# Optimization experiments

Hardware: AMD Instinct MI355X
Metric: run time of the kernel (lower is better)

The kernel has to match this reference:

```python
import jax, jax.numpy as jnp
import numpy as np

WINDOW = 4  # window_size
H = 8       # n_heads


def setup_inputs() -> dict:
    key = jax.random.key(0)
    ks = jax.random.split(key, 12)
    B, C, T = 4, 512, 1024
    d = C // H
    x = jax.random.normal(ks[0], (B, C, T), dtype=jnp.float32)
    mask = jnp.ones((B, 1, 1, T), dtype=jnp.int32)
    s = 0.02
    Wq = jax.random.normal(ks[1], (C, C), dtype=jnp.float32) * s
    Wk = jax.random.normal(ks[2], (C, C), dtype=jnp.float32) * s
    Wv = jax.random.normal(ks[3], (C, C), dtype=jnp.float32) * s
    Wo = jax.random.normal(ks[4], (C, C), dtype=jnp.float32) * s
    bq = jnp.zeros((C,), jnp.float32)
    bk = jnp.zeros((C,), jnp.float32)
    bv = jnp.zeros((C,), jnp.float32)
    bo = jnp.zeros((C,), jnp.float32)
    rel_std = d ** (-0.5)
    emb_rel_k = jax.random.normal(ks[5], (1, 2 * WINDOW + 1, d), dtype=jnp.float32) * rel_std
    emb_rel_v = jax.random.normal(ks[6], (1, 2 * WINDOW + 1, d), dtype=jnp.float32) * rel_std
    return {"x": x, "mask": mask, "Wq": Wq, "bq": bq, "Wk": Wk, "bk": bk,
            "Wv": Wv, "bv": bv, "Wo": Wo, "bo": bo,
            "emb_rel_k": emb_rel_k, "emb_rel_v": emb_rel_v}


def _slice_rel_emb(emb, T, pad_len, start, end):
    # F.pad(emb, [0,0,pad,pad,0,0]) then [:, start:end] -> [1, 2T-1, d]
    p = jnp.pad(emb, ((0, 0), (pad_len, pad_len), (0, 0)))
    return p[:, start:end]


def reference(x, mask, Wq, bq, Wk, bk, Wv, bv, Wo, bo, emb_rel_k, emb_rel_v):
    B, C, T = x.shape
    d = C // H
    scale = jnp.asarray(np.sqrt(d), x.dtype)

    def proj(Wm, bm):
        return jnp.einsum('oc,bct->bot', Wm, x) + bm[None, :, None]

    def to_heads(t):  # [B,C,T] -> [B,H,T,d]
        return t.reshape(B, H, d, T).transpose(0, 1, 3, 2)

    query = to_heads(proj(Wq, bq))
    key_ = to_heads(proj(Wk, bk))
    value = to_heads(proj(Wv, bv))

    score = jnp.einsum('bhtd,bhsd->bhts', query, key_) / scale

    pad_len = max(0, T - (WINDOW + 1))
    start = max(0, WINDOW + 1 - T)
    end = start + 2 * T - 1

    k_emb = _slice_rel_emb(emb_rel_k, T, pad_len, start, end)  # [1, 2T-1, d]
    rel = jnp.einsum('bhtd,rd->bhtr', query, k_emb[0])          # [B,H,T,2T-1]
    # skew trick: relative -> absolute
    rel = jnp.pad(rel, ((0, 0), (0, 0), (0, 0), (0, 1))).reshape(B, H, 2 * T * T)
    rel = jnp.pad(rel, ((0, 0), (0, 0), (0, T - 1))).reshape(B, H, T + 1, 2 * T - 1)
    score_loc = rel[:, :, :T, T - 1:] / scale
    score = score + score_loc

    score = jnp.where(mask == 0, jnp.asarray(-10000.0, score.dtype), score)
    p_attn = jax.nn.softmax(score, axis=-1)  # dropout=0 (eval)

    output = jnp.einsum('bhts,bhsd->bhtd', p_attn, value)

    # inverse skew: absolute -> relative weights [B,H,T,2T-1]
    pw = jnp.pad(p_attn, ((0, 0), (0, 0), (0, 0), (0, T - 1))).reshape(B, H, T * (2 * T - 1))
    pw = jnp.pad(pw, ((0, 0), (0, 0), (T, 0))).reshape(B, H, T, 2 * T)[:, :, :, 1:]
    v_emb = _slice_rel_emb(emb_rel_v, T, pad_len, start, end)  # [1, 2T-1, d]
    output = output + jnp.einsum('bhtr,rd->bhtd', pw, v_emb[0])

    out = output.transpose(0, 1, 3, 2).reshape(B, C, T)
    return jnp.einsum('oc,bct->bot', Wo, out) + bo[None, :, None]
```

## Files before the change

### kernel.cpp

```cpp
#include <hip/hip_runtime.h>

typedef unsigned short u16;
typedef unsigned int u32;
using f32x4 = __attribute__((ext_vector_type(4))) float;
using s16x8 = __attribute__((ext_vector_type(8))) short;
using u16x4 = __attribute__((ext_vector_type(4))) unsigned short;
using u16x8 = __attribute__((ext_vector_type(8))) unsigned short;

#define GLOAD_LDS16(g, s)                                     \
  __builtin_amdgcn_global_load_lds(                           \
      (const __attribute__((address_space(1))) void*)(g),     \
      (__attribute__((address_space(3))) void*)(s), 16, 0, 0)

namespace {

constexpr int T = 1024;
constexpr int C = 512;
constexpr float QSCALE = 0.125f * 1.4426950408889634f;
constexpr float MASKED = -14427.0f;
constexpr float DEFER_THR = 11.0f;

__device__ inline u16 f2bf(float f) {
  u32 u = __builtin_bit_cast(u32, f);
  u32 r = (u + 0x7fffu + ((u >> 16) & 1u)) >> 16;
  return (u16)r;
}
__device__ inline float bf2f(u16 v) {
  return __builtin_bit_cast(float, (u32)v << 16);
}
__device__ inline f32x4 mfma16(s16x8 a, s16x8 b, f32x4 c) {
  return __builtin_amdgcn_mfma_f32_16x16x32_bf16(a, b, c, 0, 0, 0);
}
__device__ inline u32 cvtpk(float lo, float hi) {
  u32 r;
  asm("v_cvt_pk_bf16_f32 %0, %1, %2" : "=v"(r) : "v"(lo), "v"(hi));
  return r;
}

__global__ __launch_bounds__(256) void convert_all(
    const float* __restrict__ x, const float* __restrict__ Wq,
    const float* __restrict__ Wk, const float* __restrict__ Wv,
    const float* __restrict__ Wo, u16* __restrict__ xb, u16* __restrict__ Wqb,
    u16* __restrict__ Wkb, u16* __restrict__ Wvb, u16* __restrict__ Wob) {
  const int tid = threadIdx.x;
  const int bid = blockIdx.x;
  const float* src;
  u16* dst;
  size_t off;
  if (bid < 2048) {
    src = x; dst = xb;
    off = ((size_t)bid * 256 + tid) * 4;
  } else {
    const int j = bid - 2048;
    const int w = j >> 8;
    src = w == 0 ? Wq : w == 1 ? Wk : w == 2 ? Wv : Wo;
    dst = w == 0 ? Wqb : w == 1 ? Wkb : w == 2 ? Wvb : Wob;
    off = (((size_t)(j & 255)) * 256 + tid) * 4;
  }
  const float4 v = *reinterpret_cast<const float4*>(src + off);
  u16x4 o;
  o[0] = f2bf(v.x); o[1] = f2bf(v.y); o[2] = f2bf(v.z); o[3] = f2bf(v.w);
  *reinterpret_cast<u16x4*>(dst + off) = o;
}

__global__ __launch_bounds__(256) void qkv_gemm(
    const u16* __restrict__ xb, const u16* __restrict__ Wqb,
    const u16* __restrict__ Wkb, const u16* __restrict__ Wvb,
    const float* __restrict__ bq, const float* __restrict__ bk,
    const float* __restrict__ bv, u16* __restrict__ qb, u16* __restrict__ kswz,
    u16* __restrict__ vswz) {
  __shared__ u16 Bs[2][128 * 32];
  __shared__ float sbias[64];
  const int tid = threadIdx.x;
  const int z = blockIdx.z;
  const int b = z / 3, wsel = z - 3 * b;
  const u16* W = wsel == 0 ? Wqb : wsel == 1 ? Wkb : Wvb;
  const float* bias = wsel == 0 ? bq : wsel == 1 ? bk : bv;
  const int o0 = blockIdx.y * 64;
  const int t0 = blockIdx.x * 128;
  if (tid < 16)
    *reinterpret_cast<float4*>(&sbias[tid * 4]) =
        *reinterpret_cast<const float4*>(&bias[o0 + tid * 4]);

  const int l = tid & 63, wid = tid >> 6;
  const int wm = wid >> 1, wn = wid & 1;
  const int lr = l & 15, lg = l >> 4;

  const int cpair = tid & 15, tgrp = tid >> 4;
  const u16* xrow =
      xb + ((size_t)(b * C) + 2 * cpair) * T + t0 + 8 * tgrp;

  const u16* Arow0 = W + (size_t)(o0 + 32 * wm + lr) * C + 8 * lg;
  const u16* Arow1 = Arow0 + 16 * C;

  f32x4 acc[2][4] = {};

  auto stage = [&](int kk, int buf) {
    const u16* p = xrow + (size_t)kk * 32 * T;
    const u16x8 v0 = *reinterpret_cast<const u16x8*>(p);
    const u16x8 v1 = *reinterpret_cast<const u16x8*>(p + T);
    char* base = (char*)&Bs[buf][0];
#pragma unroll
    for (int j = 0; j < 8; ++j) {
      const int t = 8 * tgrp + j;
      const u32 w2 = (u32)v0[j] | ((u32)v1[j] << 16);
      *(u32*)(base + ((t * 64 + 4 * cpair) ^ ((t & 3) << 4))) = w2;
    }
  };

  s16x8 a0 = *reinterpret_cast<const s16x8*>(Arow0);
  s16x8 a1 = *reinterpret_cast<const s16x8*>(Arow1);
  stage(0, 0);
  __syncthreads();

  for (int kk = 0; kk < 16; ++kk) {
    s16x8 an0, an1;
    if (kk < 15) {
      an0 = *reinterpret_cast<const s16x8*>(Arow0 + (kk + 1) * 32);
      an1 = *reinterpret_cast<const s16x8*>(Arow1 + (kk + 1) * 32);
      stage(kk + 1, (kk + 1) & 1);
    }
    const char* rb = (const char*)&Bs[kk & 1][0];
#pragma unroll
    for (int nf = 0; nf < 4; ++nf) {
      const int t = 64 * wn + 16 * nf + lr;
      const s16x8 bfrag = *reinterpret_cast<const s16x8*>(
          rb + ((t * 64 + 16 * lg) ^ ((t & 3) << 4)));
      acc[0][nf] = mfma16(a0, bfrag, acc[0][nf]);
      acc[1][nf] = mfma16(a1, bfrag, acc[1][nf]);
    }
    __syncthreads();
    if (kk < 15) { a0 = an0; a1 = an1; }
  }

  const int h = o0 >> 6;
  const size_t bh = (size_t)(b * 8 + h);
  if (wsel == 0) {
#pragma unroll
    for (int m = 0; m < 2; ++m) {
      const int ob = 32 * wm + 16 * m + 4 * lg;
#pragma unroll
      for (int nf = 0; nf < 4; ++nf) {
        const int t = t0 + 64 * wn + 16 * nf + lr;
        u16x4 pk;
#pragma unroll
        for (int r = 0; r < 4; ++r)
          pk[r] = f2bf((acc[m][nf][r] + sbias[ob + r]) * QSCALE);
        *reinterpret_cast<u16x4*>(&qb[(bh * T + t) * 64 + ob]) = pk;
      }
    }
  } else if (wsel == 1) {
    char* kbase = (char*)kswz;
#pragma unroll
    for (int m = 0; m < 2; ++m) {
      const int ob = 32 * wm + 16 * m + 4 * lg;
#pragma unroll
      for (int nf = 0; nf < 4; ++nf) {
        const int t = t0 + 64 * wn + 16 * nf + lr;
        const int tile = t >> 6, row = t & 63;
        u16x4 pk;
#pragma unroll
        for (int r = 0; r < 4; ++r) pk[r] = f2bf(acc[m][nf][r] + sbias[ob + r]);
        const int off = (row * 128 + 2 * ob) ^ ((row & 7) << 4);
        *(u16x4*)(kbase + (bh * 16 + tile) * 8192 + off) = pk;
      }
    }
  } else {
    char* vbase = (char*)vswz;
#pragma unroll
    for (int m = 0; m < 2; ++m) {
      const int ob = 32 * wm + 16 * m + 4 * lg;
#pragma unroll
      for (int nf = 0; nf < 4; ++nf) {
        const int t = t0 + 64 * wn + 16 * nf + lr;
        const int tile = t >> 6, col2 = 2 * (t & 63);
#pragma unroll
        for (int r = 0; r < 4; ++r) {
          const int dd = ob + r;
          const int off = (dd * 128 + col2) ^ ((dd & 7) << 4);
          *(u16*)(vbase + (bh * 16 + tile) * 8192 + off) =
              f2bf(acc[m][nf][r] + sbias[dd]);
        }
      }
    }
  }
}

__global__ __launch_bounds__(512) void attn_swapped(
    const u16* __restrict__ qb, const u16* __restrict__ kswz,
    const u16* __restrict__ vswz, const int* __restrict__ gmask,
    const float* __restrict__ ek, const float* __restrict__ ev,
    u16* __restrict__ op0, u16* __restrict__ op1, float2* __restrict__ mlb) {
  __shared__ u16 Kbuf[2][8192];
  __shared__ u16 Vbuf[2][8192];
  __shared__ u16 Pdiag[8][256];
  __shared__ float rkk[128][12];
  __shared__ float eks[9][64];
  __shared__ float evs[9][64];
  __shared__ u16 zerobuf[16];
  __shared__ int tflag[16];

  const int z = blockIdx.z;
  const int b = z >> 1, shalf = z & 1;
  const int h = blockIdx.y, tc = blockIdx.x * 128;
  const int tid = threadIdx.x;
  const int l = tid & 63, wid = tid >> 6;
  const int lr = l & 15, lg = l >> 4;

  const size_t bh = (size_t)(b * 8 + h);
  const u16* qbh = qb + bh * T * 64;
  const u16* kimg0 = kswz + bh * 65536;
  const u16* vimg0 = vswz + bh * 65536;

  if (tid < 144) {
    reinterpret_cast<float4*>(&eks[0][0])[tid] =
        reinterpret_cast<const float4*>(ek)[tid];
    reinterpret_cast<float4*>(&evs[0][0])[tid] =
        reinterpret_cast<const float4*>(ev)[tid];
  }
  if (tid < 16) { tflag[tid] = 1; zerobuf[tid] = 0; }
  __syncthreads();

  auto stage_pair = [&](int stp, int buf) {
    const u16* ki = kimg0 + (size_t)stp * 4096;
    const u16* vi = vimg0 + (size_t)stp * 4096;
#pragma unroll
    for (int j = 0; j < 2; ++j) {
      const int seg = wid + 8 * j;
      GLOAD_LDS16(ki + seg * 512 + l * 8, &Kbuf[buf][seg * 512]);
      GLOAD_LDS16(vi + seg * 512 + l * 8, &Vbuf[buf][seg * 512]);
    }
  };
  const int st0 = shalf * 8;
  stage_pair(st0, 0);

  if (tid < 256) {
    const int4 mm = reinterpret_cast<const int4*>(gmask + b * T)[tid];
    if (!(mm.x && mm.y && mm.z && mm.w)) tflag[tid >> 4] = 0;
  }

  {
    const int r = tid >> 2, sub = tid & 3;
    const u16* qp = qbh + (size_t)(tc + r) * 64 + sub * 16;
    const u16x8 q0 = *reinterpret_cast<const u16x8*>(qp);
    const u16x8 q1 = *reinterpret_cast<const u16x8*>(qp + 8);
    float qf[16];
#pragma unroll
    for (int j = 0; j < 8; ++j) {
      qf[j] = bf2f(q0[j]);
      qf[j + 8] = bf2f(q1[j]);
    }
    float part[9];
#pragma unroll
    for (int w = 0; w < 9; ++w) {
      float s = 0.f;
      const float* er = &eks[w][sub * 16];
#pragma unroll
      for (int d = 0; d < 16; ++d) s += qf[d] * er[d];
      part[w] = s;
    }
#pragma unroll
    for (int w = 0; w < 9; ++w) {
      part[w] += __shfl_xor(part[w], 1);
      part[w] += __shfl_xor(part[w], 2);
    }
    if (sub == 0) {
#pragma unroll
      for (int w = 0; w < 9; ++w) rkk[r][w] = part[w];
    }
  }

  const int tbw = tc + 16 * wid;
  const int qg = tbw + lr;
  s16x8 aq0, aq1;
  {
    const u16* qgp = qbh + (size_t)qg * 64;
    aq0 = *reinterpret_cast<const s16x8*>(qgp + 8 * lg);
    aq1 = *reinterpret_cast<const s16x8*>(qgp + 32 + 8 * lg);
  }

  s16x8 evA[4];
#pragma unroll
  for (int nf = 0; nf < 4; ++nf) {
    const int dd = 16 * nf + lr;
#pragma unroll
    for (int e = 0; e < 8; ++e) {
      float v = 0.f;
      if (lg == 0) v = evs[e][dd];
      else if (lg == 1 && e == 0) v = evs[8][dd];
      evA[nf][e] = (short)f2bf(v);
    }
  }

  float m = -1e30f, lsum = 0.f;
  f32x4 Oa[4] = {};
  u16* Pd = &Pdiag[wid][0];

  __syncthreads();

  auto redist = [&](const f32x4* St, s16x8& pv0, s16x8& pv1) {
    u32 wpk[4][2];
#pragma unroll
    for (int nf = 0; nf < 4; ++nf) {
      wpk[nf][0] = cvtpk(St[nf][0], St[nf][1]);
      wpk[nf][1] = cvtpk(St[nf][2], St[nf][3]);
    }
    const int srcLo = lr + ((lg & 1) << 5);
    const int srcHi = srcLo + 16;
    const bool hiSel = (lg >> 1) != 0;
    union { u32 u[4]; s16x8 v; } pa0, pa1;
    {
      const u32 a0_ = __shfl((int)wpk[0][0], srcLo), b0_ = __shfl((int)wpk[1][0], srcLo);
      const u32 a1_ = __shfl((int)wpk[0][1], srcLo), b1_ = __shfl((int)wpk[1][1], srcLo);
      const u32 a2_ = __shfl((int)wpk[0][0], srcHi), b2_ = __shfl((int)wpk[1][0], srcHi);
      const u32 a3_ = __shfl((int)wpk[0][1], srcHi), b3_ = __shfl((int)wpk[1][1], srcHi);
      pa0.u[0] = hiSel ? b0_ : a0_; pa0.u[1] = hiSel ? b1_ : a1_;
      pa0.u[2] = hiSel ? b2_ : a2_; pa0.u[3] = hiSel ? b3_ : a3_;
    }
    {
      const u32 a0_ = __shfl((int)wpk[2][0], srcLo), b0_ = __shfl((int)wpk[3][0], srcLo);
      const u32 a1_ = __shfl((int)wpk[2][1], srcLo), b1_ = __shfl((int)wpk[3][1], srcLo);
      const u32 a2_ = __shfl((int)wpk[2][0], srcHi), b2_ = __shfl((int)wpk[3][0], srcHi);
      const u32 a3_ = __shfl((int)wpk[2][1], srcHi), b3_ = __shfl((int)wpk[3][1], srcHi);
      pa1.u[0] = hiSel ? b0_ : a0_; pa1.u[1] = hiSel ? b1_ : a1_;
      pa1.u[2] = hiSel ? b2_ : a2_; pa1.u[3] = hiSel ? b3_ : a3_;
    }
    pv0 = pa0.v;
    pv1 = pa1.v;
  };

  int cur = 0;
  for (int ii = 0; ii < 4; ++ii) {
    const int stp = st0 + 2 * ii;
    const int s0 = stp * 64, s1 = s0 + 64;
    if (ii < 3) stage_pair(stp + 2, cur ^ 1);

    f32x4 StA[4] = {}, StB[4] = {};
    const char* ksb = (const char*)&Kbuf[cur][0];
#pragma unroll
    for (int nf = 0; nf < 4; ++nf) {
      const int srow = 16 * nf + lr;
      const int swz = (srow & 7) << 4;
      const int o0_ = (srow * 128 + 16 * lg) ^ swz;
      const int o1_ = (srow * 128 + 16 * (lg + 4)) ^ swz;
      const s16x8 ka0 = *reinterpret_cast<const s16x8*>(ksb + o0_);
      const s16x8 ka1 = *reinterpret_cast<const s16x8*>(ksb + o1_);
      const s16x8 kb0 = *reinterpret_cast<const s16x8*>(ksb + 8192 + o0_);
      const s16x8 kb1 = *reinterpret_cast<const s16x8*>(ksb + 8192 + o1_);
      StA[nf] = mfma16(ka0, aq0, StA[nf]);
      StB[nf] = mfma16(kb0, aq0, StB[nf]);
      StA[nf] = mfma16(ka1, aq1, StA[nf]);
      StB[nf] = mfma16(kb1, aq1, StB[nf]);
    }

    const bool diagA = (s0 <= tbw + 19) && (s0 + 63 >= tbw - 4);
    const bool diagB = (s1 <= tbw + 19) && (s1 + 63 >= tbw - 4);

    if (diagA) {
#pragma unroll
      for (int nf = 0; nf < 4; ++nf)
#pragma unroll
        for (int r = 0; r < 4; ++r) {
          const int sd = (s0 + 16 * nf + 4 * lg + r) - qg;
          if (sd >= -4 && sd <= 4) StA[nf][r] += rkk[16 * wid + lr][sd + 4];
        }
    }
    if (diagB) {
#pragma unroll
      for (int nf = 0; nf < 4; ++nf)
#pragma unroll
        for (int r = 0; r < 4; ++r) {
          const int sd = (s1 + 16 * nf + 4 * lg + r) - qg;
          if (sd >= -4 && sd <= 4) StB[nf][r] += rkk[16 * wid + lr][sd + 4];
        }
    }
    if (!tflag[stp]) {
#pragma unroll
      for (int nf = 0; nf < 4; ++nf)
#pragma unroll
        for (int r = 0; r < 4; ++r)
          if (gmask[b * T + s0 + 16 * nf + 4 * lg + r] == 0) StA[nf][r] = MASKED;
    }
    if (!tflag[stp + 1]) {
#pragma unroll
      for (int nf = 0; nf < 4; ++nf)
#pragma unroll
        for (int r = 0; r < 4; ++r)
          if (gmask[b * T + s1 + 16 * nf + 4 * lg + r] == 0) StB[nf][r] = MASKED;
    }

    float rm;
    {
      float mv = fmaxf(fmaxf(StA[0][0], StA[0][1]), fmaxf(StA[0][2], StA[0][3]));
#pragma unroll
      for (int nf = 1; nf < 4; ++nf)
        mv = fmaxf(mv, fmaxf(fmaxf(StA[nf][0], StA[nf][1]),
                             fmaxf(StA[nf][2], StA[nf][3])));
#pragma unroll
      for (int nf = 0; nf < 4; ++nf)
        mv = fmaxf(mv, fmaxf(fmaxf(StB[nf][0], StB[nf][1]),
                             fmaxf(StB[nf][2], StB[nf][3])));
      rm = mv;
      rm = fmaxf(rm, __shfl_xor(rm, 16));
      rm = fmaxf(rm, __shfl_xor(rm, 32));
    }
    if (!__all(rm - m <= DEFER_THR)) {
      const float mn = fmaxf(m, rm);
      const float corr = exp2f(m - mn);
#pragma unroll
      for (int nf = 0; nf < 4; ++nf) {
        Oa[nf][0] *= corr; Oa[nf][1] *= corr;
        Oa[nf][2] *= corr; Oa[nf][3] *= corr;
      }
      lsum *= corr;
      m = mn;
    }
    float rs = 0.f;
#pragma unroll
    for (int nf = 0; nf < 4; ++nf)
#pragma unroll
      for (int r = 0; r < 4; ++r) {
        const float pA = exp2f(StA[nf][r] - m);
        const float pB = exp2f(StB[nf][r] - m);
        StA[nf][r] = pA;
        StB[nf][r] = pB;
        rs += pA + pB;
      }
    rs += __shfl_xor(rs, 16);
    rs += __shfl_xor(rs, 32);
    lsum += rs;

    const bool diagP = diagA || diagB;
    if (diagP) {
      u32* pz = (u32*)Pd;
      pz[l] = 0; pz[l + 64] = 0;
      if (diagA) {
#pragma unroll
        for (int nf = 0; nf < 4; ++nf)
#pragma unroll
          for (int r = 0; r < 4; ++r) {
            const int sd = (s0 + 16 * nf + 4 * lg + r) - qg;
            if (sd >= -4 && sd <= 4) Pd[lr * 16 + sd + 4] = f2bf(StA[nf][r]);
          }
      }
      if (diagB) {
#pragma unroll
        for (int nf = 0; nf < 4; ++nf)
#pragma unroll
          for (int r = 0; r < 4; ++r) {
            const int sd = (s1 + 16 * nf + 4 * lg + r) - qg;
            if (sd >= -4 && sd <= 4) Pd[lr * 16 + sd + 4] = f2bf(StB[nf][r]);
          }
      }
    }

    const char* vsb = (const char*)&Vbuf[cur][0];
    {
      s16x8 pa0, pa1;
      redist(StA, pa0, pa1);
#pragma unroll
      for (int nf = 0; nf < 4; ++nf) {
        const int dd = 16 * nf + lr;
        const int swz = (dd & 7) << 4;
        const s16x8 bv0 = *reinterpret_cast<const s16x8*>(
            vsb + ((dd * 128 + 16 * lg) ^ swz));
        const s16x8 bv1 = *reinterpret_cast<const s16x8*>(
            vsb + ((dd * 128 + 16 * (lg + 4)) ^ swz));
        Oa[nf] = mfma16(bv0, pa0, Oa[nf]);
        Oa[nf] = mfma16(bv1, pa1, Oa[nf]);
      }
    }
    {
      s16x8 pa0, pa1;
      redist(StB, pa0, pa1);
#pragma unroll
      for (int nf = 0; nf < 4; ++nf) {
        const int dd = 16 * nf + lr;
        const int swz = (dd & 7) << 4;
        const s16x8 bv0 = *reinterpret_cast<const s16x8*>(
            vsb + 8192 + ((dd * 128 + 16 * lg) ^ swz));
        const s16x8 bv1 = *reinterpret_cast<const s16x8*>(
            vsb + 8192 + ((dd * 128 + 16 * (lg + 4)) ^ swz));
        Oa[nf] = mfma16(bv0, pa0, Oa[nf]);
        Oa[nf] = mfma16(bv1, pa1, Oa[nf]);
      }
    }

    if (diagP) {
      const u16* pdsrc = (lg < 2) ? &Pd[lr * 16 + 8 * lg] : &zerobuf[0];
      const s16x8 pd = *reinterpret_cast<const s16x8*>(pdsrc);
#pragma unroll
      for (int nf = 0; nf < 4; ++nf) Oa[nf] = mfma16(evA[nf], pd, Oa[nf]);
    }

    __syncthreads();
    cur ^= 1;
  }

  u16* op = shalf ? op1 : op0;
#pragma unroll
  for (int nf = 0; nf < 4; ++nf) {
    u16x4 pk;
#pragma unroll
    for (int r = 0; r < 4; ++r) pk[r] = f2bf(Oa[nf][r]);
    *reinterpret_cast<u16x4*>(
        &op[(bh * T + qg) * 64 + 16 * nf + 4 * lg]) = pk;
  }
  if (lg == 0) {
    float2 v;
    v.x = m;
    v.y = lsum;
    mlb[(size_t)shalf * 32768 + bh * T + qg] = v;
  }
}

__global__ __launch_bounds__(256) void merge_halves(
    const u16* __restrict__ op0, const u16* __restrict__ op1,
    const float2* __restrict__ mlb, u16* __restrict__ attb) {
  const int tid = threadIdx.x;
  const int row = blockIdx.x * 16 + (tid >> 4);
  const int dd = (tid & 15) * 4;
  const float2 ml0 = mlb[row];
  const float2 ml1 = mlb[32768 + row];
  const float mm = fmaxf(ml0.x, ml1.x);
  const float a0 = exp2f(ml0.x - mm), a1 = exp2f(ml1.x - mm);
  const float inv = 1.0f / (a0 * ml0.y + a1 * ml1.y);
  const u16x4 v0 = *reinterpret_cast<const u16x4*>(&op0[(size_t)row * 64 + dd]);
  const u16x4 v1 = *reinterpret_cast<const u16x4*>(&op1[(size_t)row * 64 + dd]);
  u16x4 o;
#pragma unroll
  for (int j = 0; j < 4; ++j)
    o[j] = f2bf((bf2f(v0[j]) * a0 + bf2f(v1[j]) * a1) * inv);
  *reinterpret_cast<u16x4*>(&attb[(size_t)row * 64 + dd]) = o;
}

__global__ __launch_bounds__(256) void out_gemm(
    const u16* __restrict__ Wob, const float* __restrict__ bo,
    const u16* __restrict__ attb, float* __restrict__ out) {
  __shared__ u16 Bs[2][128 * 32];
  __shared__ float sbias[64];
  const int tid = threadIdx.x;
  const int b = blockIdx.z;
  const int o0 = blockIdx.y * 64;
  const int t0 = blockIdx.x * 128;
  if (tid < 16)
    *reinterpret_cast<float4*>(&sbias[tid * 4]) =
        *reinterpret_cast<const float4*>(&bo[o0 + tid * 4]);

  const int l = tid & 63, wid = tid >> 6;
  const int wm = wid >> 1, wn = wid & 1;
  const int lr = l & 15, lg = l >> 4;

  const int slot = tid & 3, trow = tid >> 2;
  const u16* Arow0 = Wob + (size_t)(o0 + 32 * wm + lr) * C + 8 * lg;
  const u16* Arow1 = Arow0 + 16 * C;

  f32x4 acc[2][4] = {};

  auto stage = [&](int kk, int buf) {
    const int c0 = kk * 32;
    const int h = c0 >> 6, dd0 = c0 & 63;
    char* base = (char*)&Bs[buf][0];
#pragma unroll
    for (int rep = 0; rep < 2; ++rep) {
      const int t = rep * 64 + trow;
      const u16x8 v = *reinterpret_cast<const u16x8*>(
          &attb[((size_t)((b * 8 + h) * T) + t0 + t) * 64 + dd0 + 8 * slot]);
      *(u16x8*)(base + ((t * 64 + 16 * slot) ^ ((t & 3) << 4))) = v;
    }
  };

  s16x8 a0 = *reinterpret_cast<const s16x8*>(Arow0);
  s16x8 a1 = *reinterpret_cast<const s16x8*>(Arow1);
  stage(0, 0);
  __syncthreads();

  for (int kk = 0; kk < 16; ++kk) {
    s16x8 an0, an1;
    if (kk < 15) {
      an0 = *reinterpret_cast<const s16x8*>(Arow0 + (kk + 1) * 32);
      an1 = *reinterpret_cast<const s16x8*>(Arow1 + (kk + 1) * 32);
      stage(kk + 1, (kk + 1) & 1);
    }
    const char* rb = (const char*)&Bs[kk & 1][0];
#pragma unroll
    for (int nf = 0; nf < 4; ++nf) {
      const int t = 64 * wn + 16 * nf + lr;
      const s16x8 bfrag = *reinterpret_cast<const s16x8*>(
          rb + ((t * 64 + 16 * lg) ^ ((t & 3) << 4)));
      acc[0][nf] = mfma16(a0, bfrag, acc[0][nf]);
      acc[1][nf] = mfma16(a1, bfrag, acc[1][nf]);
    }
    __syncthreads();
    if (kk < 15) { a0 = an0; a1 = an1; }
  }

#pragma unroll
  for (int m = 0; m < 2; ++m) {
    const int ol = 32 * wm + 16 * m + 4 * lg;
#pragma unroll
    for (int nf = 0; nf < 4; ++nf) {
      const int t = t0 + 64 * wn + 16 * nf + lr;
#pragma unroll
      for (int r = 0; r < 4; ++r)
        out[((size_t)(b * C) + o0 + ol + r) * T + t] =
            acc[m][nf][r] + sbias[ol + r];
    }
  }
}

}

extern "C" void kernel_launch(void* const* d_in, const int* in_sizes, int n_in,
                              void* d_out, int out_size, void* d_ws,
                              size_t ws_size, hipStream_t stream) {
  const float* x    = (const float*)d_in[0];
  const int*   mask = (const int*)d_in[1];
  const float* Wq   = (const float*)d_in[2];
  const float* bq   = (const float*)d_in[3];
  const float* Wk   = (const float*)d_in[4];
  const float* bk   = (const float*)d_in[5];
  const float* Wv   = (const float*)d_in[6];
  const float* bv   = (const float*)d_in[7];
  const float* Wo   = (const float*)d_in[8];
  const float* bo   = (const float*)d_in[9];
  const float* ek   = (const float*)d_in[10];
  const float* ev   = (const float*)d_in[11];
  float* out = (float*)d_out;

  char* ws = (char*)d_ws;
  u16* xb   = (u16*)(ws);
  u16* Wqb  = (u16*)(ws + 4194304);
  u16* Wkb  = (u16*)(ws + 4718592);
  u16* Wvb  = (u16*)(ws + 5242880);
  u16* Wob  = (u16*)(ws + 5767168);
  u16* qb   = (u16*)(ws + 6291456);
  u16* kswz = (u16*)(ws + 10485760);
  u16* vswz = (u16*)(ws + 14680064);
  u16* attb = (u16*)(ws + 18874368);
  u16* op0  = xb;
  u16* op1  = (u16*)(ws + 23068672);
  float2* mlb = (float2*)(ws + 27262976);

  convert_all<<<dim3(3072), dim3(256), 0, stream>>>(x, Wq, Wk, Wv, Wo, xb, Wqb,
                                                    Wkb, Wvb, Wob);
  qkv_gemm<<<dim3(8, 8, 12), dim3(256), 0, stream>>>(xb, Wqb, Wkb, Wvb, bq, bk,
                                                     bv, qb, kswz, vswz);
  attn_swapped<<<dim3(8, 8, 8), dim3(512), 0, stream>>>(
      qb, kswz, vswz, mask, ek, ev, op0, op1, mlb);
  merge_halves<<<dim3(2048), dim3(256), 0, stream>>>(op0, op1, mlb, attb);
  out_gemm<<<dim3(8, 8, 4), dim3(256), 0, stream>>>(Wob, bo, attb, out);
}
```

Baseline: 81.92 us.

## Permute V layout to drop P shuffle redistribution, add setprio, shrink out_gemm tiles

The V image columns are now stored in a permuted order, so the softmax P accumulator fragments can be packed directly as MFMA operands with swapped operand order. This removes the per-tile cross-lane shuffle redistribution. The rescale correction is now shuffled per row to match the transposed output layout, and the output store becomes scalar. It also raises wave priority around the MFMA blocks and halves the out_gemm tile width to launch twice as many blocks. The cost is a more intricate layout coupling between the QKV and attention kernels, plus less coalesced output stores.

```diff
diff --git a/kernel.cpp b/kernel.cpp
--- a/kernel.cpp
+++ b/kernel.cpp
@@ -173,11 +173,13 @@
 #pragma unroll
       for (int nf = 0; nf < 4; ++nf) {
         const int t = t0 + 64 * wn + 16 * nf + lr;
-        const int tile = t >> 6, col2 = 2 * (t & 63);
+        const int tile = t >> 6, s_ = t & 63;
+        const int sp = 32 * (s_ >> 5) + 8 * ((s_ & 15) >> 2) +
+                       4 * ((s_ >> 4) & 1) + (s_ & 3);
 #pragma unroll
         for (int r = 0; r < 4; ++r) {
           const int dd = ob + r;
-          const int off = (dd * 128 + col2) ^ ((dd & 7) << 4);
+          const int off = (dd * 128 + 2 * sp) ^ ((dd & 7) << 4);
           *(u16*)(vbase + (bh * 16 + tile) * 8192 + off) =
               f2bf(acc[m][nf][r] + sbias[dd]);
         }
@@ -197,7 +199,6 @@
   __shared__ float rkk[128][12];
   __shared__ float eks[9][64];
   __shared__ float evs[9][64];
-  __shared__ u16 zerobuf[16];
   __shared__ int tflag[16];
 
   const int z = blockIdx.z;
@@ -218,7 +219,7 @@
     reinterpret_cast<float4*>(&evs[0][0])[tid] =
         reinterpret_cast<const float4*>(ev)[tid];
   }
-  if (tid < 16) { tflag[tid] = 1; zerobuf[tid] = 0; }
+  if (tid < 16) tflag[tid] = 1;
   __syncthreads();
 
   auto stage_pair = [&](int stp, int buf) {
@@ -298,37 +299,6 @@
 
   __syncthreads();
 
-  auto redist = [&](const f32x4* St, s16x8& pv0, s16x8& pv1) {
-    u32 wpk[4][2];
-#pragma unroll
-    for (int nf = 0; nf < 4; ++nf) {
-      wpk[nf][0] = cvtpk(St[nf][0], St[nf][1]);
-      wpk[nf][1] = cvtpk(St[nf][2], St[nf][3]);
-    }
-    const int srcLo = lr + ((lg & 1) << 5);
-    const int srcHi = srcLo + 16;
-    const bool hiSel = (lg >> 1) != 0;
-    union { u32 u[4]; s16x8 v; } pa0, pa1;
-    {
-      const u32 a0_ = __shfl((int)wpk[0][0], srcLo), b0_ = __shfl((int)wpk[1][0], srcLo);
-      const u32 a1_ = __shfl((int)wpk[0][1], srcLo), b1_ = __shfl((int)wpk[1][1], srcLo);
-      const u32 a2_ = __shfl((int)wpk[0][0], srcHi), b2_ = __shfl((int)wpk[1][0], srcHi);
-      const u32 a3_ = __shfl((int)wpk[0][1], srcHi), b3_ = __shfl((int)wpk[1][1], srcHi);
-      pa0.u[0] = hiSel ? b0_ : a0_; pa0.u[1] = hiSel ? b1_ : a1_;
-      pa0.u[2] = hiSel ? b2_ : a2_; pa0.u[3] = hiSel ? b3_ : a3_;
-    }
-    {
-      const u32 a0_ = __shfl((int)wpk[2][0], srcLo), b0_ = __shfl((int)wpk[3][0], srcLo);
-      const u32 a1_ = __shfl((int)wpk[2][1], srcLo), b1_ = __shfl((int)wpk[3][1], srcLo);
-      const u32 a2_ = __shfl((int)wpk[2][0], srcHi), b2_ = __shfl((int)wpk[3][0], srcHi);
-      const u32 a3_ = __shfl((int)wpk[2][1], srcHi), b3_ = __shfl((int)wpk[3][1], srcHi);
-      pa1.u[0] = hiSel ? b0_ : a0_; pa1.u[1] = hiSel ? b1_ : a1_;
-      pa1.u[2] = hiSel ? b2_ : a2_; pa1.u[3] = hiSel ? b3_ : a3_;
-    }
-    pv0 = pa0.v;
-    pv1 = pa1.v;
-  };
-
   int cur = 0;
   for (int ii = 0; ii < 4; ++ii) {
     const int stp = st0 + 2 * ii;
@@ -337,6 +307,7 @@
 
     f32x4 StA[4] = {}, StB[4] = {};
     const char* ksb = (const char*)&Kbuf[cur][0];
+    __builtin_amdgcn_s_setprio(1);
 #pragma unroll
     for (int nf = 0; nf < 4; ++nf) {
       const int srow = 16 * nf + lr;
@@ -352,6 +323,7 @@
       StA[nf] = mfma16(ka1, aq1, StA[nf]);
       StB[nf] = mfma16(kb1, aq1, StB[nf]);
     }
+    __builtin_amdgcn_s_setprio(0);
 
     const bool diagA = (s0 <= tbw + 19) && (s0 + 63 >= tbw - 4);
     const bool diagB = (s1 <= tbw + 19) && (s1 + 63 >= tbw - 4);
@@ -407,10 +379,14 @@
     if (!__all(rm - m <= DEFER_THR)) {
       const float mn = fmaxf(m, rm);
       const float corr = exp2f(m - mn);
+      const float c0 = __shfl(corr, 4 * lg + 0);
+      const float c1 = __shfl(corr, 4 * lg + 1);
+      const float c2 = __shfl(corr, 4 * lg + 2);
+      const float c3 = __shfl(corr, 4 * lg + 3);
 #pragma unroll
       for (int nf = 0; nf < 4; ++nf) {
-        Oa[nf][0] *= corr; Oa[nf][1] *= corr;
-        Oa[nf][2] *= corr; Oa[nf][3] *= corr;
+        Oa[nf][0] *= c0; Oa[nf][1] *= c1;
+        Oa[nf][2] *= c2; Oa[nf][3] *= c3;
       }
       lsum *= corr;
       m = mn;
@@ -430,6 +406,24 @@
     rs += __shfl_xor(rs, 32);
     lsum += rs;
 
+    union { u32 u[4]; s16x8 v; } paA0, paA1, paB0, paB1;
+    paA0.u[0] = cvtpk(StA[0][0], StA[0][1]);
+    paA0.u[1] = cvtpk(StA[0][2], StA[0][3]);
+    paA0.u[2] = cvtpk(StA[1][0], StA[1][1]);
+    paA0.u[3] = cvtpk(StA[1][2], StA[1][3]);
+    paA1.u[0] = cvtpk(StA[2][0], StA[2][1]);
+    paA1.u[1] = cvtpk(StA[2][2], StA[2][3]);
+    paA1.u[2] = cvtpk(StA[3][0], StA[3][1]);
+    paA1.u[3] = cvtpk(StA[3][2], StA[3][3]);
+    paB0.u[0] = cvtpk(StB[0][0], StB[0][1]);
+    paB0.u[1] = cvtpk(StB[0][2], StB[0][3]);
+    paB0.u[2] = cvtpk(StB[1][0], StB[1][1]);
+    paB0.u[3] = cvtpk(StB[1][2], StB[1][3]);
+    paB1.u[0] = cvtpk(StB[2][0], StB[2][1]);
+    paB1.u[1] = cvtpk(StB[2][2], StB[2][3]);
+    paB1.u[2] = cvtpk(StB[3][0], StB[3][1]);
+    paB1.u[3] = cvtpk(StB[3][2], StB[3][3]);
+
     const bool diagP = diagA || diagB;
     if (diagP) {
       u32* pz = (u32*)Pd;
@@ -455,42 +449,30 @@
     }
 
     const char* vsb = (const char*)&Vbuf[cur][0];
-    {
-      s16x8 pa0, pa1;
-      redist(StA, pa0, pa1);
-#pragma unroll
-      for (int nf = 0; nf < 4; ++nf) {
-        const int dd = 16 * nf + lr;
-        const int swz = (dd & 7) << 4;
-        const s16x8 bv0 = *reinterpret_cast<const s16x8*>(
-            vsb + ((dd * 128 + 16 * lg) ^ swz));
-        const s16x8 bv1 = *reinterpret_cast<const s16x8*>(
-            vsb + ((dd * 128 + 16 * (lg + 4)) ^ swz));
-        Oa[nf] = mfma16(bv0, pa0, Oa[nf]);
-        Oa[nf] = mfma16(bv1, pa1, Oa[nf]);
-      }
-    }
-    {
-      s16x8 pa0, pa1;
-      redist(StB, pa0, pa1);
-#pragma unroll
-      for (int nf = 0; nf < 4; ++nf) {
-        const int dd = 16 * nf + lr;
-        const int swz = (dd & 7) << 4;
-        const s16x8 bv0 = *reinterpret_cast<const s16x8*>(
-            vsb + 8192 + ((dd * 128 + 16 * lg) ^ swz));
-        const s16x8 bv1 = *reinterpret_cast<const s16x8*>(
-            vsb + 8192 + ((dd * 128 + 16 * (lg + 4)) ^ swz));
-        Oa[nf] = mfma16(bv0, pa0, Oa[nf]);
-        Oa[nf] = mfma16(bv1, pa1, Oa[nf]);
-      }
-    }
+    __builtin_amdgcn_s_setprio(1);
+#pragma unroll
+    for (int nf = 0; nf < 4; ++nf) {
+      const int dd = 16 * nf + lr;
+      const int swz = (dd & 7) << 4;
+      const int o0_ = (dd * 128 + 16 * lg) ^ swz;
+      const int o1_ = (dd * 128 + 16 * (lg + 4)) ^ swz;
+      const s16x8 bv0 = *reinterpret_cast<const s16x8*>(vsb + o0_);
+      const s16x8 bv1 = *reinterpret_cast<const s16x8*>(vsb + o1_);
+      const s16x8 cv0 = *reinterpret_cast<const s16x8*>(vsb + 8192 + o0_);
+      const s16x8 cv1 = *reinterpret_cast<const s16x8*>(vsb + 8192 + o1_);
+      Oa[nf] = mfma16(paA0.v, bv0, Oa[nf]);
+      Oa[nf] = mfma16(paA1.v, bv1, Oa[nf]);
+      Oa[nf] = mfma16(paB0.v, cv0, Oa[nf]);
+      Oa[nf] = mfma16(paB1.v, cv1, Oa[nf]);
+    }
+    __builtin_amdgcn_s_setprio(0);
 
     if (diagP) {
-      const u16* pdsrc = (lg < 2) ? &Pd[lr * 16 + 8 * lg] : &zerobuf[0];
-      const s16x8 pd = *reinterpret_cast<const s16x8*>(pdsrc);
-#pragma unroll
-      for (int nf = 0; nf < 4; ++nf) Oa[nf] = mfma16(evA[nf], pd, Oa[nf]);
+      s16x8 pdv = {};
+      if (lg < 2)
+        pdv = *reinterpret_cast<const s16x8*>(&Pd[lr * 16 + 8 * lg]);
+#pragma unroll
+      for (int nf = 0; nf < 4; ++nf) Oa[nf] = mfma16(pdv, evA[nf], Oa[nf]);
     }
 
     __syncthreads();
@@ -499,13 +481,10 @@
 
   u16* op = shalf ? op1 : op0;
 #pragma unroll
-  for (int nf = 0; nf < 4; ++nf) {
-    u16x4 pk;
-#pragma unroll
-    for (int r = 0; r < 4; ++r) pk[r] = f2bf(Oa[nf][r]);
-    *reinterpret_cast<u16x4*>(
-        &op[(bh * T + qg) * 64 + 16 * nf + 4 * lg]) = pk;
-  }
+  for (int nf = 0; nf < 4; ++nf)
+#pragma unroll
+    for (int r = 0; r < 4; ++r)
+      op[(bh * T + tbw + 4 * lg + r) * 64 + 16 * nf + lr] = f2bf(Oa[nf][r]);
   if (lg == 0) {
     float2 v;
     v.x = m;
@@ -537,12 +516,12 @@
 __global__ __launch_bounds__(256) void out_gemm(
     const u16* __restrict__ Wob, const float* __restrict__ bo,
     const u16* __restrict__ attb, float* __restrict__ out) {
-  __shared__ u16 Bs[2][128 * 32];
+  __shared__ u16 Bs[2][64 * 32];
   __shared__ float sbias[64];
   const int tid = threadIdx.x;
   const int b = blockIdx.z;
   const int o0 = blockIdx.y * 64;
-  const int t0 = blockIdx.x * 128;
+  const int t0 = blockIdx.x * 64;
   if (tid < 16)
     *reinterpret_cast<float4*>(&sbias[tid * 4]) =
         *reinterpret_cast<const float4*>(&bo[o0 + tid * 4]);
@@ -555,19 +534,15 @@
   const u16* Arow0 = Wob + (size_t)(o0 + 32 * wm + lr) * C + 8 * lg;
   const u16* Arow1 = Arow0 + 16 * C;
 
-  f32x4 acc[2][4] = {};
+  f32x4 acc[2][2] = {};
 
   auto stage = [&](int kk, int buf) {
     const int c0 = kk * 32;
     const int h = c0 >> 6, dd0 = c0 & 63;
     char* base = (char*)&Bs[buf][0];
-#pragma unroll
-    for (int rep = 0; rep < 2; ++rep) {
-      const int t = rep * 64 + trow;
-      const u16x8 v = *reinterpret_cast<const u16x8*>(
-          &attb[((size_t)((b * 8 + h) * T) + t0 + t) * 64 + dd0 + 8 * slot]);
-      *(u16x8*)(base + ((t * 64 + 16 * slot) ^ ((t & 3) << 4))) = v;
-    }
+    const u16x8 v = *reinterpret_cast<const u16x8*>(
+        &attb[((size_t)((b * 8 + h) * T) + t0 + trow) * 64 + dd0 + 8 * slot]);
+    *(u16x8*)(base + ((trow * 64 + 16 * slot) ^ ((trow & 3) << 4))) = v;
   };
 
   s16x8 a0 = *reinterpret_cast<const s16x8*>(Arow0);
@@ -584,8 +559,8 @@
     }
     const char* rb = (const char*)&Bs[kk & 1][0];
 #pragma unroll
-    for (int nf = 0; nf < 4; ++nf) {
-      const int t = 64 * wn + 16 * nf + lr;
+    for (int nf = 0; nf < 2; ++nf) {
+      const int t = 32 * wn + 16 * nf + lr;
       const s16x8 bfrag = *reinterpret_cast<const s16x8*>(
           rb + ((t * 64 + 16 * lg) ^ ((t & 3) << 4)));
       acc[0][nf] = mfma16(a0, bfrag, acc[0][nf]);
@@ -599,8 +574,8 @@
   for (int m = 0; m < 2; ++m) {
     const int ol = 32 * wm + 16 * m + 4 * lg;
 #pragma unroll
-    for (int nf = 0; nf < 4; ++nf) {
-      const int t = t0 + 64 * wn + 16 * nf + lr;
+    for (int nf = 0; nf < 2; ++nf) {
+      const int t = t0 + 32 * wn + 16 * nf + lr;
 #pragma unroll
       for (int r = 0; r < 4; ++r)
         out[((size_t)(b * C) + o0 + ol + r) * T + t] =
@@ -649,5 +624,5 @@
   attn_swapped<<<dim3(8, 8, 8), dim3(512), 0, stream>>>(
       qb, kswz, vswz, mask, ek, ev, op0, op1, mlb);
   merge_halves<<<dim3(2048), dim3(256), 0, stream>>>(op0, op1, mlb, attb);
-  out_gemm<<<dim3(8, 8, 4), dim3(256), 0, stream>>>(Wob, bo, attb, out);
-}
+  out_gemm<<<dim3(16, 8, 4), dim3(256), 0, stream>>>(Wob, bo, attb, out);
+}
```

Result: slower. 88.90 us (+8.5%).
